# Kernel tuning notes

Hardware: AMD Instinct MI355X
Metric: run time of the kernel (lower is better)

The kernel has to match this reference:

```python
import jax, jax.numpy as jnp
import numpy as np

N_CONTEXT = 8
N_ANS = 8


def _g_mlp(x, Wg1, bg1, Wg2, bg2, Wg3, bg3):
    # 3-layer relation MLP G, applied per object pair
    h = jax.nn.relu(x @ Wg1 + bg1)
    h = jax.nn.relu(h @ Wg2 + bg2)
    return jax.nn.relu(h @ Wg3 + bg3)


def setup_inputs() -> dict:
    key = jax.random.key(0)
    ks = jax.random.split(key, 12)
    B, P, C, H, W = 512, 16, 1, 80, 80
    D = 512                      # embedding_dim
    T = 2 * (D + 9)              # object_tuple_size = 1042
    s = jnp.float32(0.02)
    f32 = jnp.float32
    return {
        "x": jax.random.normal(ks[0], (B, P, C, H, W), f32),
        "W_emb": jax.random.normal(ks[1], (C * H * W, D), f32) * s,
        "b_emb": jnp.zeros((D,), f32),
        "Wg1": jax.random.normal(ks[2], (T, T), f32) * s,
        "bg1": jnp.zeros((T,), f32),
        "Wg2": jax.random.normal(ks[3], (T, T), f32) * s,
        "bg2": jnp.zeros((T,), f32),
        "Wg3": jax.random.normal(ks[4], (T, T), f32) * s,
        "bg3": jnp.zeros((T,), f32),
        "Wf1": jax.random.normal(ks[5], (T, T), f32) * s,
        "bf1": jnp.zeros((T,), f32),
        "Wf2": jax.random.normal(ks[6], (T, 1), f32) * s,
        "bf2": jnp.zeros((1,), f32),
        "labels_idx": jax.random.randint(ks[7], (B,), 0, N_ANS),
    }


def reference(x, W_emb, b_emb, Wg1, bg1, Wg2, bg2, Wg3, bg3,
              Wf1, bf1, Wf2, bf2, labels_idx):
    B = x.shape[0]
    D = W_emb.shape[1]
    # frozen embedding (torch.no_grad) -> stop_gradient
    emb = jax.lax.stop_gradient(
        x.reshape(B * (N_CONTEXT + N_ANS), -1) @ W_emb + b_emb
    ).reshape(B, N_CONTEXT + N_ANS, D)

    # TagPanelEmbeddings: context panels -> one-hot 0..7, answers -> one-hot 8 (9 dims)
    eye9 = jnp.eye(9, dtype=emb.dtype)
    tags = jnp.concatenate([eye9[:N_CONTEXT],
                            jnp.tile(eye9[8:9], (N_ANS, 1))], axis=0)  # (16, 9)
    tagged = jnp.concatenate(
        [emb, jnp.broadcast_to(tags, (B, N_CONTEXT + N_ANS, 9))], axis=-1)  # (B,16,D+9)

    ctx = tagged[:, :N_CONTEXT]   # (B,8,d)
    cho = tagged[:, N_CONTEXT:]   # (B,8,d)
    d = ctx.shape[-1]

    # all 8x8 ordered context pairs: pair[i,j] = concat(obj_j, obj_i)
    ctx_pairs = jnp.concatenate([
        jnp.broadcast_to(ctx[:, None, :, :], (B, 8, 8, d)),
        jnp.broadcast_to(ctx[:, :, None, :], (B, 8, 8, d)),
    ], axis=-1).reshape(B, 64, 2 * d)
    ctx_g = _g_mlp(ctx_pairs, Wg1, bg1, Wg2, bg2, Wg3, bg3).sum(axis=1)  # (B,T)

    # context-choice pairs, vectorized over all 8 answers:
    # pair[a,k] = concat(context_k, choice_a)  -> (B, N_ANS, 8, 2d)
    cc_pairs = jnp.concatenate([
        jnp.broadcast_to(ctx[:, None, :, :], (B, N_ANS, 8, d)),
        jnp.broadcast_to(cho[:, :, None, :], (B, N_ANS, 8, d)),
    ], axis=-1)
    cc_g = _g_mlp(cc_pairs, Wg1, bg1, Wg2, bg2, Wg3, bg3).sum(axis=2)  # (B,N_ANS,T)

    relations = ctx_g[:, None, :] + cc_g  # (B,N_ANS,T); norm = Identity

    # F readout: 2-layer MLP to scalar per answer
    h = jax.nn.relu(relations @ Wf1 + bf1)
    f_out = (h @ Wf2 + bf2)[..., 0]  # (B, N_ANS)

    labels = jax.nn.one_hot(labels_idx, N_ANS, dtype=f_out.dtype)
    # stable BCE-with-logits, mean over all elements
    loss = jnp.mean(jnp.maximum(f_out, 0) - f_out * labels
                    + jnp.log1p(jnp.exp(-jnp.abs(f_out))))
    preds = jnp.argmax(f_out, axis=1)
    acc = jnp.mean((preds == labels_idx).astype(f_out.dtype))
    return loss, acc
```

## Files before the change

### kernel.cpp

```cpp
#include <hip/hip_runtime.h>
#include <hip/hip_bf16.h>
#include <math.h>


typedef __bf16 bf16;
typedef __bf16 v8bf __attribute__((ext_vector_type(8)));
typedef float  v4f  __attribute__((ext_vector_type(4)));
typedef unsigned long long u64;

#define GAS(p) ((const __attribute__((address_space(1))) void*)(p))
#define LAS(p) ((__attribute__((address_space(3))) void*)(p))

__global__ __launch_bounds__(256) void gemm_bf16(
    const bf16* __restrict__ A, int lda,
    const bf16* __restrict__ Bt, int ldb,
    bf16* __restrict__ C, int ldc,
    int Mt, int Nt,
    int Nreal, int Nstore, int K,
    const float* __restrict__ bias,
    const float* __restrict__ tagW, int tag_ld,
    int relu, int mode)
{
    __shared__ bf16 As[128 * 32];
    __shared__ bf16 Bs[128 * 32];
    __shared__ bf16 Epi[64 * 132];

    const int L    = blockIdx.x;
    const int xcd  = L & 7;
    const int idx  = L >> 3;
    const int mlee = idx / Nt;
    const int n    = idx - mlee * Nt;
    const int m    = xcd * (Mt >> 3) + mlee;
    const int row0 = m * 128;
    const int col0 = n * 128;

    const int tid  = threadIdx.x;
    const int wv   = tid >> 6;
    const int lane = tid & 63;
    const int quad = lane >> 4;
    const int l15  = lane & 15;
    const int wm0  = (wv >> 1) * 64;
    const int wn0  = (wv & 1) * 64;

    v4f acc[4][4] = {};

    const int srow  = wv * 32 + (lane >> 2);
    const int skoff = (lane & 3) * 8;
    const bf16* ga = A  + (size_t)(row0 + srow) * lda + skoff;
    const bf16* gb = Bt + (size_t)(col0 + srow) * ldb + skoff;
    bf16* laA = &As[(wv * 32) * 32];
    bf16* laB = &Bs[(wv * 32) * 32];

    for (int k0 = 0; k0 < K; k0 += 32) {
        __builtin_amdgcn_global_load_lds(GAS(ga),                    LAS(laA),           16, 0, 0);
        __builtin_amdgcn_global_load_lds(GAS(ga + (size_t)16 * lda), LAS(laA + 16 * 32), 16, 0, 0);
        __builtin_amdgcn_global_load_lds(GAS(gb),                    LAS(laB),           16, 0, 0);
        __builtin_amdgcn_global_load_lds(GAS(gb + (size_t)16 * ldb), LAS(laB + 16 * 32), 16, 0, 0);
        ga += 32; gb += 32;
        __syncthreads();

        v8bf af[4], bfq[4];
        #pragma unroll
        for (int i = 0; i < 4; ++i)
            af[i] = *(const v8bf*)&As[(wm0 + i * 16 + l15) * 32 + quad * 8];
        #pragma unroll
        for (int j = 0; j < 4; ++j)
            bfq[j] = *(const v8bf*)&Bs[(wn0 + j * 16 + l15) * 32 + quad * 8];
        #pragma unroll
        for (int i = 0; i < 4; ++i)
            #pragma unroll
            for (int j = 0; j < 4; ++j)
                acc[i][j] = __builtin_amdgcn_mfma_f32_16x16x32_bf16(af[i], bfq[j], acc[i][j], 0, 0, 0);
        __syncthreads();
    }

    float bcol[4];
    #pragma unroll
    for (int j = 0; j < 4; ++j) {
        int col = col0 + wn0 + j * 16 + l15;
        bcol[j] = (col < Nreal && bias) ? bias[col] : 0.f;
    }

    float s_ctx = 0.f;

    #pragma unroll
    for (int pass = 0; pass < 2; ++pass) {
        if (wm0 == pass * 64) {
            #pragma unroll
            for (int i = 0; i < 4; ++i) {
                #pragma unroll
                for (int j = 0; j < 4; ++j) {
                    #pragma unroll
                    for (int r = 0; r < 4; ++r) {
                        int lrow = i * 16 + quad * 4 + r;
                        int lcol = wn0 + j * 16 + l15;
                        int col  = col0 + lcol;
                        float v = 0.f;
                        if (col < Nreal) {
                            v = acc[i][j][r] + bcol[j];
                            if (tagW) {
                                int row = row0 + pass * 64 + lrow;
                                int tp = row & 15; if (tp > 8) tp = 8;
                                v += tagW[(size_t)tp * tag_ld + col];
                            }
                            if (relu) v = fmaxf(v, 0.f);
                        }
                        Epi[lrow * 132 + lcol] = (bf16)v;
                    }
                }
            }
        }
        __syncthreads();

        if (mode == 0) {
            int lrow = tid >> 2;
            int cg   = (tid & 3) * 32;
            int grow = row0 + pass * 64 + lrow;
            #pragma unroll
            for (int k = 0; k < 4; ++k) {
                int c = cg + k * 8;
                int gcol = col0 + c;
                if (gcol < Nstore) {
                    u64 q0 = *(const u64*)&Epi[lrow * 132 + c];
                    u64 q1 = *(const u64*)&Epi[lrow * 132 + c + 4];
                    uint4 st;
                    st.x = (unsigned)q0; st.y = (unsigned)(q0 >> 32);
                    st.z = (unsigned)q1; st.w = (unsigned)(q1 >> 32);
                    *(uint4*)&C[(size_t)grow * ldc + gcol] = st;
                }
            }
        } else {
            if (tid < 128) {
                int col = tid;
                if (pass == 0) {
                    float s = 0.f;
                    for (int r = 0; r < 64; ++r) s += (float)Epi[r * 132 + col];
                    s_ctx = s;
                } else {
                    float sA[8] = {};
                    for (int r = 0; r < 64; ++r) sA[r >> 3] += (float)Epi[r * 132 + col];
                    int gcol = col0 + col;
                    if (gcol < Nstore) {
                        #pragma unroll
                        for (int a = 0; a < 8; ++a)
                            C[(size_t)(m * 8 + a) * ldc + gcol] = (bf16)(s_ctx + sA[a]);
                    }
                }
            }
        }
        __syncthreads();
    }
}

template<int AMODE, int CMODE>
__global__ __launch_bounds__(512, 2) void gemm256(
    const bf16* __restrict__ A, int lda,
    const bf16* __restrict__ U, const bf16* __restrict__ V, int lduv,
    const bf16* __restrict__ Bt, int ldb,
    bf16* __restrict__ C, int ldc,
    int Mt, int Nt, int Nreal, int Nstore, int K,
    const float* __restrict__ bias)
{
    extern __shared__ char smem[];

    const int NTK = K >> 6;

    const int L    = blockIdx.x;
    const int xcd  = L & 7;
    const int idx  = L >> 3;
    const int mlee = idx / Nt;
    const int n    = idx - mlee * Nt;
    const int m    = xcd * (Mt >> 3) + mlee;
    const int row0 = m * 256;
    const int col0 = n * 256;

    const int tid  = threadIdx.x;
    const int wv   = tid >> 6;
    const int lane = tid & 63;
    const int wr   = wv >> 2;
    const int wc   = wv & 3;
    const int l15  = lane & 15;
    const int quad = lane >> 4;
    const int s7   = l15 & 7;
    const int slot0 = ((0 + quad) ^ s7) << 4;
    const int slot1 = ((4 + quad) ^ s7) << 4;

    char* const aRd = smem + wr * 16384;
    char* const bRd = smem + 65536 + (wc >> 1) * 16384 + (wc & 1) * 8192;

    const int srow = tid >> 3;
    const int sl   = tid & 7;
    const int gce  = (sl ^ (srow & 7)) * 8;
    const bf16* const Ab = (AMODE == 0 ? A : U) + (size_t)(row0 + srow) * (AMODE == 0 ? lda : 0) + gce;
    const bf16* const Bb = Bt + (size_t)(col0 + srow) * ldb + gce;

#define STAGE_A(kt, bo, h) { \
    const bf16* s_ = Ab + (size_t)((h) * 128) * lda + (kt) * 64; \
    char* d_ = smem + (bo) + (h) * 16384 + wv * 1024; \
    __builtin_amdgcn_global_load_lds(GAS(s_),                    LAS(d_),        16, 0, 0); \
    __builtin_amdgcn_global_load_lds(GAS(s_ + (size_t)64 * lda), LAS(d_ + 8192), 16, 0, 0); }
#define STAGE_B(kt, bo, h) { \
    const bf16* s_ = Bb + (size_t)((h) * 128) * ldb + (kt) * 64; \
    char* d_ = smem + 65536 + (bo) + (h) * 16384 + wv * 1024; \
    __builtin_amdgcn_global_load_lds(GAS(s_),                    LAS(d_),        16, 0, 0); \
    __builtin_amdgcn_global_load_lds(GAS(s_ + (size_t)64 * ldb), LAS(d_ + 8192), 16, 0, 0); }

#define LDA4(bo, qmB) \
    _Pragma("unroll") \
    for (int i_ = 0; i_ < 4; ++i_) { \
        afr[i_][0] = *(const v8bf*)(aRd + (bo) + (((qmB) + i_) * 16 + l15) * 128 + slot0); \
        afr[i_][1] = *(const v8bf*)(aRd + (bo) + (((qmB) + i_) * 16 + l15) * 128 + slot1); \
    }
#define LDB2(bo, nfB) \
    _Pragma("unroll") \
    for (int j_ = 0; j_ < 2; ++j_) { \
        bfr[(nfB) + j_][0] = *(const v8bf*)(bRd + (bo) + (((nfB) + j_) * 16 + l15) * 128 + slot0); \
        bfr[(nfB) + j_][1] = *(const v8bf*)(bRd + (bo) + (((nfB) + j_) * 16 + l15) * 128 + slot1); \
    }
#define MM8(qmA, nfB) \
    _Pragma("unroll") \
    for (int i_ = 0; i_ < 4; ++i_) \
        _Pragma("unroll") \
        for (int j_ = 0; j_ < 2; ++j_) { \
            acc[(qmA) + i_][(nfB) + j_] = __builtin_amdgcn_mfma_f32_16x16x32_bf16(afr[i_][0], bfr[(nfB) + j_][0], acc[(qmA) + i_][(nfB) + j_], 0, 0, 0); \
            acc[(qmA) + i_][(nfB) + j_] = __builtin_amdgcn_mfma_f32_16x16x32_bf16(afr[i_][1], bfr[(nfB) + j_][1], acc[(qmA) + i_][(nfB) + j_], 0, 0, 0); \
        }
#define UVLOAD(uu, vv, h, t1) { \
    uu[0] = *(const v8bf*)(U + uo[h][0] + (t1) * 64); \
    vv[0] = *(const v8bf*)(V + vo[h][0] + (t1) * 64); \
    uu[1] = *(const v8bf*)(U + uo[h][1] + (t1) * 64); \
    vv[1] = *(const v8bf*)(V + vo[h][1] + (t1) * 64); }
#define WRITEA(uu, vv, bo, h) { \
    _Pragma("unroll") \
    for (int q_ = 0; q_ < 2; ++q_) { \
        v8bf o_; \
        _Pragma("unroll") \
        for (int e_ = 0; e_ < 8; ++e_) \
            o_[e_] = (bf16)fmaxf((float)uu[q_][e_] + (float)vv[q_][e_], 0.f); \
        *(v8bf*)(smem + (bo) + (h) * 16384 + (q_ * 64 + srow) * 128 + ((sl ^ (srow & 7)) << 4)) = o_; \
    } }
#define BAR()   asm volatile("s_barrier" ::: "memory")
#define FENCE() asm volatile("s_waitcnt vmcnt(0) lgkmcnt(0)" ::: "memory")
#define PRIO1() __builtin_amdgcn_s_setprio(1)
#define PRIO0() __builtin_amdgcn_s_setprio(0)

    v4f acc[8][4] = {};
    v8bf afr[4][2], bfr[4][2];
    v8bf u0[2], v0[2], u1[2], v1[2];
    int uo[2][2], vo[2][2];

    if constexpr (AMODE == 1) {
        #pragma unroll
        for (int h = 0; h < 2; ++h)
            #pragma unroll
            for (int q = 0; q < 2; ++q) {
                int gr = row0 + h * 128 + q * 64 + srow;
                int bb = gr >> 7, p = gr & 127;
                uo[h][q] = (bb * 16 + (p & 7)) * lduv + sl * 8;
                vo[h][q] = (bb * 16 + (p >> 3)) * lduv + sl * 8;
            }
    }

    if constexpr (AMODE == 0) {
        STAGE_A(0, 0, 0); STAGE_A(0, 0, 1);
    } else {
        UVLOAD(u0, v0, 0, 0); UVLOAD(u1, v1, 1, 0);
    }
    STAGE_B(0, 0, 0); STAGE_B(0, 0, 1);
    if constexpr (AMODE == 1) {
        WRITEA(u0, v0, 0, 0); WRITEA(u1, v1, 0, 1);
    }
    FENCE();
    BAR();

    for (int t = 0; t < NTK; ++t) {
        const int bo = (t & 1) << 15;
        const int no = bo ^ 32768;
        const bool hn = (t + 1 < NTK);
        LDA4(bo, 0); LDB2(bo, 0);
        if constexpr (AMODE == 0) { if (hn) STAGE_A(t + 1, no, 0); }
        BAR(); PRIO1(); MM8(0, 0); PRIO0(); BAR();
        LDB2(bo, 2);
        if (hn) {
            if constexpr (AMODE == 1) { UVLOAD(u0, v0, 0, t + 1); }
            else                      { STAGE_A(t + 1, no, 1); }
            STAGE_B(t + 1, no, 0);
        }
        BAR(); PRIO1(); MM8(0, 2); PRIO0(); BAR();
        LDA4(bo, 4);
        if (hn) {
            if constexpr (AMODE == 1) { UVLOAD(u1, v1, 1, t + 1); WRITEA(u0, v0, no, 0); }
            STAGE_B(t + 1, no, 1);
        }
        BAR(); PRIO1(); MM8(4, 0); PRIO0(); BAR();
        if (hn) {
            if constexpr (AMODE == 1) { WRITEA(u1, v1, no, 1); }
        }
        FENCE();
        BAR(); PRIO1(); MM8(4, 2); PRIO0(); BAR();
    }

    if constexpr (CMODE == 0) {
        __syncthreads();
        bf16* epi = (bf16*)(smem + wv * 16384);
        #pragma unroll
        for (int j = 0; j < 4; ++j) {
            int col = col0 + wc * 64 + j * 16 + l15;
            bool real = col < Nreal;
            float bc = (real && bias) ? bias[col] : 0.f;
            #pragma unroll
            for (int i = 0; i < 8; ++i) {
                #pragma unroll
                for (int r = 0; r < 4; ++r) {
                    int lrow = i * 16 + quad * 4 + r;
                    float v = real ? fmaxf(acc[i][j][r] + bc, 0.f) : 0.f;
                    int slt = (j * 2 + (l15 >> 3)) ^ (lrow & 7);
                    epi[(lrow * 128 + (slt << 4) + ((l15 & 7) << 1)) >> 1] = (bf16)v;
                }
            }
        }
        #pragma unroll
        for (int it = 0; it < 16; ++it) {
            int lrow = it * 8 + (lane >> 3);
            int cb   = lane & 7;
            v8bf vv = *(const v8bf*)&epi[(lrow * 128 + ((cb ^ (lrow & 7)) << 4)) >> 1];
            int grow = row0 + wr * 128 + lrow;
            int gcol = col0 + wc * 64 + cb * 8;
            if (gcol < Nstore)
                *(v8bf*)&C[(size_t)grow * ldc + gcol] = vv;
        }
    } else {
        const int ccol = col0 + wc * 64 + l15;
        const int bb = (row0 >> 7) + wr;
        #pragma unroll
        for (int j = 0; j < 4; ++j) {
            int col = ccol + j * 16;
            bool real = col < Nreal;
            float bc = (real && bias) ? bias[col] : 0.f;
            float red[9];
            float sc = 0.f;
            #pragma unroll
            for (int i = 0; i < 4; ++i)
                #pragma unroll
                for (int r = 0; r < 4; ++r)
                    sc += fmaxf(acc[i][j][r] + bc, 0.f);
            red[0] = sc;
            #pragma unroll
            for (int a = 0; a < 8; ++a) {
                float s = 0.f;
                if ((quad >> 1) == (a & 1)) {
                    const int i = 4 + (a >> 1);
                    #pragma unroll
                    for (int r = 0; r < 4; ++r)
                        s += fmaxf(acc[i][j][r] + bc, 0.f);
                }
                red[1 + a] = s;
            }
            #pragma unroll
            for (int k = 0; k < 9; ++k) {
                red[k] += __shfl_xor(red[k], 16, 64);
                red[k] += __shfl_xor(red[k], 32, 64);
            }
            if (quad == 0 && col < Nstore) {
                #pragma unroll
                for (int a = 0; a < 8; ++a)
                    C[(size_t)(bb * 8 + a) * ldc + col] = (bf16)(red[0] + red[1 + a]);
            }
        }
    }
#undef STAGE_A
#undef STAGE_B
#undef LDA4
#undef LDB2
#undef MM8
#undef UVLOAD
#undef WRITEA
#undef BAR
#undef FENCE
#undef PRIO1
#undef PRIO0
}

__global__ void transpose_cast(const float* __restrict__ W, int ldw,
                               int krows, int ncols,
                               bf16* __restrict__ Bt, int ldb,
                               int nalloc, int kalloc)
{
    __shared__ float t[32][33];
    int kb = blockIdx.x * 32;
    int nb = blockIdx.y * 32;
    int tx = threadIdx.x, ty = threadIdx.y;
    #pragma unroll
    for (int i = 0; i < 4; ++i) {
        int k = kb + ty + i * 8, n = nb + tx;
        t[ty + i * 8][tx] = (k < krows && n < ncols) ? W[(size_t)k * ldw + n] : 0.f;
    }
    __syncthreads();
    #pragma unroll
    for (int i = 0; i < 4; ++i) {
        int n = nb + ty + i * 8, k = kb + tx;
        if (n < nalloc && k < kalloc)
            Bt[(size_t)n * ldb + k] = (bf16)t[tx][ty + i * 8];
    }
}

__global__ void cast_bf16_vec(const float* __restrict__ in, bf16* __restrict__ out, size_t n4)
{
    size_t i = blockIdx.x * (size_t)blockDim.x + threadIdx.x;
    if (i >= n4) return;
    float4 v = ((const float4*)in)[i];
    union { bf16 h[4]; u64 q; } o;
    o.h[0] = (bf16)v.x; o.h[1] = (bf16)v.y; o.h[2] = (bf16)v.z; o.h[3] = (bf16)v.w;
    *(u64*)&out[i * 4] = o.q;
}

__global__ void fout_kernel(const bf16* __restrict__ h, const float* __restrict__ Wf2,
                            const float* __restrict__ bf2, float* __restrict__ fout,
                            int rows, int T, int ldp)
{
    int wid  = (int)((blockIdx.x * (size_t)blockDim.x + threadIdx.x) >> 6);
    int lane = threadIdx.x & 63;
    if (wid >= rows) return;
    const bf16* hr = h + (size_t)wid * ldp;
    float s = 0.f;
    for (int c = lane; c < T; c += 64) s += (float)hr[c] * Wf2[c];
    #pragma unroll
    for (int off = 32; off > 0; off >>= 1) s += __shfl_down(s, off, 64);
    if (lane == 0) fout[wid] = s + bf2[0];
}

__global__ void loss_kernel(const float* __restrict__ fout, const int* __restrict__ labels,
                            float* __restrict__ out)
{
    __shared__ float sl[512];
    __shared__ float sc[512];
    int b = threadIdx.x;
    const float* f = fout + (size_t)b * 8;
    int lab = labels[b];
    float rl = 0.f;
    int best = 0;
    float bv = f[0];
    #pragma unroll
    for (int a = 0; a < 8; ++a) {
        float v = f[a];
        rl += fmaxf(v, 0.f) - v * ((a == lab) ? 1.f : 0.f) + log1pf(expf(-fabsf(v)));
        if (v > bv) { bv = v; best = a; }
    }
    sl[b] = rl;
    sc[b] = (best == lab) ? 1.f : 0.f;
    __syncthreads();
    for (int s = 256; s > 0; s >>= 1) {
        if (b < s) { sl[b] += sl[b + s]; sc[b] += sc[b + s]; }
        __syncthreads();
    }
    if (b == 0) { out[0] = sl[0] / 4096.f; out[1] = sc[0] / 512.f; }
}

extern "C" void kernel_launch(void* const* d_in, const int* in_sizes, int n_in,
                              void* d_out, int out_size, void* d_ws, size_t ws_size,
                              hipStream_t stream)
{
    (void)in_sizes; (void)n_in; (void)out_size;
    const float* x      = (const float*)d_in[0];
    const float* W_emb  = (const float*)d_in[1];
    const float* b_emb  = (const float*)d_in[2];
    const float* Wg1    = (const float*)d_in[3];
    const float* bg1    = (const float*)d_in[4];
    const float* Wg2    = (const float*)d_in[5];
    const float* bg2    = (const float*)d_in[6];
    const float* Wg3    = (const float*)d_in[7];
    const float* bg3    = (const float*)d_in[8];
    const float* Wf1    = (const float*)d_in[9];
    const float* bf1    = (const float*)d_in[10];
    const float* Wf2    = (const float*)d_in[11];
    const float* bf2    = (const float*)d_in[12];
    const int*   labels = (const int*)d_in[13];

    const int B = 512, S = 16, E = 6400, D = 512, T = 1042;
    const int TP  = 1088;
    const int NA  = 1152;
    const int NAB = 1280;

    static int attr_set = 0;
    if (!attr_set) {
        (void)hipFuncSetAttribute(reinterpret_cast<const void*>(&gemm256<1, 0>),
                                  hipFuncAttributeMaxDynamicSharedMemorySize, 131072);
        (void)hipFuncSetAttribute(reinterpret_cast<const void*>(&gemm256<0, 1>),
                                  hipFuncAttributeMaxDynamicSharedMemorySize, 131072);
        attr_set = 1;
    }

    auto alignup = [](size_t v) { return (v + 255) & ~(size_t)255; };

    size_t fixed = alignup((size_t)B * 8 * 4)
                 + alignup((size_t)D * E * 2)
                 + 2 * alignup((size_t)NA * D * 2)
                 + 2 * alignup((size_t)NAB * TP * 2)
                 + alignup((size_t)NA * TP * 2);

    int Bc = 512;
    for (;;) {
        size_t need = fixed
            + alignup((size_t)Bc * S * E * 2)
            + alignup((size_t)Bc * S * D * 2)
            + 2 * alignup((size_t)Bc * S * TP * 2)
            + alignup((size_t)Bc * 128 * TP * 2)
            + alignup((size_t)Bc * 8 * TP * 2)
            + alignup((size_t)Bc * 8 * TP * 2);
        if (need <= ws_size || Bc == 16) break;
        Bc >>= 1;
    }

    char* p = (char*)d_ws;
    auto take = [&](size_t bytes) -> void* {
        char* r = p; p += (bytes + 255) & ~(size_t)255; return r;
    };
    float* fout  = (float*)take((size_t)B * 8 * 4);
    bf16* W_embT = (bf16*)take((size_t)D * E * 2);
    bf16* W1aT   = (bf16*)take((size_t)NA * D * 2);
    bf16* W1bT   = (bf16*)take((size_t)NA * D * 2);
    bf16* Wg2T   = (bf16*)take((size_t)NAB * TP * 2);
    bf16* Wg3T   = (bf16*)take((size_t)NAB * TP * 2);
    bf16* Wf1T   = (bf16*)take((size_t)NA * TP * 2);
    bf16* xb     = (bf16*)take((size_t)Bc * S * E * 2);
    bf16* embB   = (bf16*)take((size_t)Bc * S * D * 2);
    bf16* Ubuf   = (bf16*)take((size_t)Bc * S * TP * 2);
    bf16* Vbuf   = (bf16*)take((size_t)Bc * S * TP * 2);
    bf16* H2     = (bf16*)take((size_t)Bc * 128 * TP * 2);
    bf16* REL    = (bf16*)take((size_t)Bc * 8 * TP * 2);
    bf16* HF     = (bf16*)take((size_t)Bc * 8 * TP * 2);

    dim3 tb(32, 8);
    transpose_cast<<<dim3(E / 32, D / 32), tb, 0, stream>>>(W_emb, D, E, D, W_embT, E, D, E);
    transpose_cast<<<dim3(D / 32, NA / 32), tb, 0, stream>>>(Wg1,                   T, D, T, W1aT, D, NA, D);
    transpose_cast<<<dim3(D / 32, NA / 32), tb, 0, stream>>>(Wg1 + (size_t)521 * T, T, D, T, W1bT, D, NA, D);
    transpose_cast<<<dim3(TP / 32, NAB / 32), tb, 0, stream>>>(Wg2, T, T, T, Wg2T, TP, NAB, TP);
    transpose_cast<<<dim3(TP / 32, NAB / 32), tb, 0, stream>>>(Wg3, T, T, T, Wg3T, TP, NAB, TP);
    transpose_cast<<<dim3(TP / 32, NA / 32), tb, 0, stream>>>(Wf1, T, T, T, Wf1T, TP, NA, TP);

    const int nch = B / Bc;
    for (int ch = 0; ch < nch; ++ch) {
        const int M1t = Bc * S / 128, M3t = Bc * 8 / 128;
        const int M2t6 = Bc * 128 / 256;

        size_t nx4 = (size_t)Bc * S * E / 4;
        cast_bf16_vec<<<(int)((nx4 + 255) / 256), 256, 0, stream>>>(
            x + (size_t)ch * Bc * S * E, xb, nx4);

        gemm_bf16<<<M1t * (D / 128), 256, 0, stream>>>(
            xb, E, W_embT, E, embB, D, M1t, D / 128, D, D, E, b_emb, nullptr, 0, 0, 0);

        gemm_bf16<<<M1t * (NA / 128), 256, 0, stream>>>(
            embB, D, W1aT, D, Ubuf, TP, M1t, NA / 128, T, TP, D, bg1, Wg1 + (size_t)512 * T, T, 0, 0);
        gemm_bf16<<<M1t * (NA / 128), 256, 0, stream>>>(
            embB, D, W1bT, D, Vbuf, TP, M1t, NA / 128, T, TP, D, nullptr, Wg1 + (size_t)1033 * T, T, 0, 0);

        gemm256<1, 0><<<M2t6 * (NAB / 256), 512, 131072, stream>>>(
            nullptr, 0, Ubuf, Vbuf, TP, Wg2T, TP, H2, TP, M2t6, NAB / 256, T, TP, TP, bg2);
        gemm256<0, 1><<<M2t6 * (NAB / 256), 512, 131072, stream>>>(
            H2, TP, nullptr, nullptr, 0, Wg3T, TP, REL, TP, M2t6, NAB / 256, T, TP, TP, bg3);

        gemm_bf16<<<M3t * (NA / 128), 256, 0, stream>>>(
            REL, TP, Wf1T, TP, HF, TP, M3t, NA / 128, T, TP, TP, bf1, nullptr, 0, 1, 0);

        fout_kernel<<<(Bc * 8 * 64 + 255) / 256, 256, 0, stream>>>(
            HF, Wf2, bf2, fout + (size_t)ch * Bc * 8, Bc * 8, T, TP);
    }

    loss_kernel<<<1, 512, 0, stream>>>(fout, labels, (float*)d_out);
}
```

Measured before the change: 1.152 ms.

## Deepen GEMM K-loop prefetch to two tiles with partial vmcnt waits

Restructures the main GEMM K-loop to prefetch two tiles ahead. Both LDS buffers are prologue-filled, the loop is unrolled by two with fixed buffer offsets, and the full vmcnt(0) fence per iteration is replaced with partial vmcnt waits. This lets global-to-LDS loads stay in flight across an iteration boundary to hide memory latency. The waits depend on exact counts of outstanding loads, so the wait counts risk being wrong and reading stale LDS data. There is also a remainder tail for odd NTK.

```diff
diff --git a/kernel.cpp b/kernel.cpp
--- a/kernel.cpp
+++ b/kernel.cpp
@@ -191,7 +191,8 @@
     const int srow = tid >> 3;
     const int sl   = tid & 7;
     const int gce  = (sl ^ (srow & 7)) * 8;
-    const bf16* const Ab = (AMODE == 0 ? A : U) + (size_t)(row0 + srow) * (AMODE == 0 ? lda : 0) + gce;
+    const bf16* const Ab = (AMODE == 0) ? A + (size_t)(row0 + srow) * lda + gce
+                                        : (const bf16*)nullptr;
     const bf16* const Bb = Bt + (size_t)(col0 + srow) * ldb + gce;
 
 #define STAGE_A(kt, bo, h) { \
@@ -240,7 +241,6 @@
         *(v8bf*)(smem + (bo) + (h) * 16384 + (q_ * 64 + srow) * 128 + ((sl ^ (srow & 7)) << 4)) = o_; \
     } }
 #define BAR()   asm volatile("s_barrier" ::: "memory")
-#define FENCE() asm volatile("s_waitcnt vmcnt(0) lgkmcnt(0)" ::: "memory")
 #define PRIO1() __builtin_amdgcn_s_setprio(1)
 #define PRIO0() __builtin_amdgcn_s_setprio(0)
 
@@ -265,39 +265,80 @@
         STAGE_A(0, 0, 0); STAGE_A(0, 0, 1);
     } else {
         UVLOAD(u0, v0, 0, 0); UVLOAD(u1, v1, 1, 0);
+        WRITEA(u0, v0, 0, 0); WRITEA(u1, v1, 0, 1);
     }
     STAGE_B(0, 0, 0); STAGE_B(0, 0, 1);
-    if constexpr (AMODE == 1) {
-        WRITEA(u0, v0, 0, 0); WRITEA(u1, v1, 0, 1);
-    }
-    FENCE();
+    if (NTK > 1) {
+        if constexpr (AMODE == 0) {
+            STAGE_A(1, 32768, 0); STAGE_A(1, 32768, 1);
+        } else {
+            UVLOAD(u0, v0, 0, 1); UVLOAD(u1, v1, 1, 1);
+            WRITEA(u0, v0, 32768, 0); WRITEA(u1, v1, 32768, 1);
+        }
+        STAGE_B(1, 32768, 0); STAGE_B(1, 32768, 1);
+    }
+    asm volatile("s_waitcnt vmcnt(0) lgkmcnt(0)" ::: "memory");
     BAR();
 
-    for (int t = 0; t < NTK; ++t) {
-        const int bo = (t & 1) << 15;
-        const int no = bo ^ 32768;
-        const bool hn = (t + 1 < NTK);
-        LDA4(bo, 0); LDB2(bo, 0);
-        if constexpr (AMODE == 0) { if (hn) STAGE_A(t + 1, no, 0); }
+    int t = 0;
+    for (; t + 1 < NTK; t += 2) {
+        const bool h2 = (t + 2 < NTK);
+        const bool h3 = (t + 3 < NTK);
+        LDA4(0, 0); LDB2(0, 0);
+        if constexpr (AMODE == 1) { if (h2) UVLOAD(u0, v0, 0, t + 2); }
         BAR(); PRIO1(); MM8(0, 0); PRIO0(); BAR();
-        LDB2(bo, 2);
-        if (hn) {
-            if constexpr (AMODE == 1) { UVLOAD(u0, v0, 0, t + 1); }
-            else                      { STAGE_A(t + 1, no, 1); }
-            STAGE_B(t + 1, no, 0);
-        }
+        LDB2(0, 2);
+        if constexpr (AMODE == 1) { if (h2) UVLOAD(u1, v1, 1, t + 2); }
         BAR(); PRIO1(); MM8(0, 2); PRIO0(); BAR();
-        LDA4(bo, 4);
-        if (hn) {
-            if constexpr (AMODE == 1) { UVLOAD(u1, v1, 1, t + 1); WRITEA(u0, v0, no, 0); }
-            STAGE_B(t + 1, no, 1);
-        }
+        LDA4(0, 4);
+        if (h2) STAGE_B(t + 2, 0, 0);
         BAR(); PRIO1(); MM8(4, 0); PRIO0(); BAR();
-        if (hn) {
-            if constexpr (AMODE == 1) { WRITEA(u1, v1, no, 1); }
-        }
-        FENCE();
-        BAR(); PRIO1(); MM8(4, 2); PRIO0(); BAR();
+        if (h2) {
+            if constexpr (AMODE == 1) { WRITEA(u0, v0, 0, 0); WRITEA(u1, v1, 0, 1); }
+            else                      { STAGE_A(t + 2, 0, 0); STAGE_A(t + 2, 0, 1); }
+        }
+        BAR(); PRIO1(); MM8(4, 2); PRIO0();
+        if constexpr (AMODE == 0) {
+            if (h2) asm volatile("s_waitcnt vmcnt(6)" ::: "memory");
+            else    asm volatile("s_waitcnt vmcnt(0)" ::: "memory");
+        } else {
+            if (h2) asm volatile("s_waitcnt vmcnt(2) lgkmcnt(0)" ::: "memory");
+            else    asm volatile("s_waitcnt vmcnt(0) lgkmcnt(0)" ::: "memory");
+        }
+        BAR();
+        LDA4(32768, 0); LDB2(32768, 0);
+        if (h2) STAGE_B(t + 2, 0, 1);
+        if constexpr (AMODE == 1) { if (h3) UVLOAD(u0, v0, 0, t + 3); }
+        BAR(); PRIO1(); MM8(0, 0); PRIO0(); BAR();
+        LDB2(32768, 2);
+        if constexpr (AMODE == 1) { if (h3) UVLOAD(u1, v1, 1, t + 3); }
+        BAR(); PRIO1(); MM8(0, 2); PRIO0(); BAR();
+        LDA4(32768, 4);
+        if (h3) STAGE_B(t + 3, 32768, 0);
+        BAR(); PRIO1(); MM8(4, 0); PRIO0(); BAR();
+        if (h3) {
+            STAGE_B(t + 3, 32768, 1);
+            if constexpr (AMODE == 1) { WRITEA(u0, v0, 32768, 0); WRITEA(u1, v1, 32768, 1); }
+            else                      { STAGE_A(t + 3, 32768, 0); STAGE_A(t + 3, 32768, 1); }
+        }
+        BAR(); PRIO1(); MM8(4, 2); PRIO0();
+        if constexpr (AMODE == 0) {
+            if (h3) asm volatile("s_waitcnt vmcnt(8)" ::: "memory");
+            else    asm volatile("s_waitcnt vmcnt(0)" ::: "memory");
+        } else {
+            if (h3) asm volatile("s_waitcnt vmcnt(4) lgkmcnt(0)" ::: "memory");
+            else    asm volatile("s_waitcnt vmcnt(0) lgkmcnt(0)" ::: "memory");
+        }
+        BAR();
+    }
+    if (t < NTK) {
+        LDA4(0, 0); LDB2(0, 0);
+        BAR(); PRIO1(); MM8(0, 0); PRIO0(); BAR();
+        LDB2(0, 2);
+        BAR(); PRIO1(); MM8(0, 2); PRIO0(); BAR();
+        LDA4(0, 4);
+        BAR(); PRIO1(); MM8(4, 0); PRIO0(); BAR();
+        PRIO1(); MM8(4, 2); PRIO0();
     }
 
     if constexpr (CMODE == 0) {
@@ -376,7 +417,6 @@
 #undef UVLOAD
 #undef WRITEA
 #undef BAR
-#undef FENCE
 #undef PRIO1
 #undef PRIO0
 }
```

After: 1.168 ms. About the same (+1.4%).
